# Kernel tuning notes

Hardware: AMD Instinct MI355X
Metric: run time of the kernel (lower is better)

Reference implementation:

```python
import jax, jax.numpy as jnp
import numpy as np

N, E, F_IN, HID, H1, H2, H3, OUT = 10000, 160000, 50, 350, 4, 4, 6, 121


def _gat(x, src, dst, n, W, a_s, a_d, b, heads, C, concat):
    # PyG GATConv (dropout=0, eval): h = xW^T reshaped to [N,H,C]
    h = (x @ W.T).reshape(n, heads, C)
    alpha_src = jnp.einsum('nhc,hc->nh', h, a_s)  # [N,H]
    alpha_dst = jnp.einsum('nhc,hc->nh', h, a_d)  # [N,H]
    e = jax.nn.leaky_relu(alpha_src[src] + alpha_dst[dst], 0.2)  # [E,H]
    # numerically-stable segment softmax over incoming edges of each dst node
    m = jax.ops.segment_max(e, dst, num_segments=n)
    ee = jnp.exp(e - m[dst])
    s = jax.ops.segment_sum(ee, dst, num_segments=n)
    alpha = ee / s[dst]  # self-loops guarantee s > 0
    out = jax.ops.segment_sum(h[src] * alpha[:, :, None], dst, num_segments=n)  # [N,H,C]
    out = out.reshape(n, heads * C) if concat else out.mean(axis=1)
    return out + b


def setup_inputs() -> dict:
    key = jax.random.key(0)
    ks = jax.random.split(key, 16)
    sc = 0.05
    inp = {
        'x': jax.random.normal(ks[0], (N, F_IN), dtype=jnp.float32),
        'edge_index': jax.random.randint(ks[1], (2, E), 0, N, dtype=jnp.int64) if jax.config.jax_enable_x64 else jax.random.randint(ks[1], (2, E), 0, N, dtype=jnp.int32),
        'W1': jax.random.normal(ks[2], (H1 * HID, F_IN), dtype=jnp.float32) * sc,
        'a1s': jax.random.normal(ks[3], (H1, HID), dtype=jnp.float32) * sc,
        'a1d': jax.random.normal(ks[4], (H1, HID), dtype=jnp.float32) * sc,
        'b1': jnp.zeros((H1 * HID,), dtype=jnp.float32),
        'W2': jax.random.normal(ks[5], (H2 * HID, H1 * HID), dtype=jnp.float32) * sc,
        'a2s': jax.random.normal(ks[6], (H2, HID), dtype=jnp.float32) * sc,
        'a2d': jax.random.normal(ks[7], (H2, HID), dtype=jnp.float32) * sc,
        'b2': jnp.zeros((H2 * HID,), dtype=jnp.float32),
        'Wskip': jax.random.normal(ks[8], (H2 * HID, H1 * HID), dtype=jnp.float32) * sc,
        'W3': jax.random.normal(ks[9], (H3 * OUT, H2 * HID), dtype=jnp.float32) * sc,
        'a3s': jax.random.normal(ks[10], (H3, OUT), dtype=jnp.float32) * sc,
        'a3d': jax.random.normal(ks[11], (H3, OUT), dtype=jnp.float32) * sc,
        'b3': jnp.zeros((OUT,), dtype=jnp.float32),
    }
    return inp


def reference(x, edge_index, W1, a1s, a1d, b1, W2, a2s, a2d, b2, Wskip, W3, a3s, a3d, b3):
    n = x.shape[0]
    loops = jnp.arange(n, dtype=edge_index.dtype)  # PyG add_self_loops=True
    src = jnp.concatenate([edge_index[0], loops])
    dst = jnp.concatenate([edge_index[1], loops])
    h = jax.nn.elu(_gat(x, src, dst, n, W1, a1s, a1d, b1, H1, HID, True))
    x_in = h
    h = jax.nn.elu(_gat(h, src, dst, n, W2, a2s, a2d, b2, H2, HID, True))
    h = h + x_in @ Wskip.T  # skip connection (bias=False)
    return _gat(h, src, dst, n, W3, a3s, a3d, b3, H3, OUT, False)
```

## Files before the change

kernel.cpp:

```cpp
#include <hip/hip_runtime.h>
#include <math.h>

#define NNODES 10000
#define NEDGES 160000
#define E2 (NEDGES + NNODES)
#define F_IN 50
#define HIDC 350
#define NH1 4
#define NH2 4
#define NH3 6
#define OUTC 121
#define MAXE 96
#define KP1 64
#define KP2 1408
#define LD3 736
#define ROWSLACK 128

typedef __attribute__((ext_vector_type(8))) short short8;
typedef __attribute__((ext_vector_type(8))) unsigned short ushort8v;
typedef __attribute__((ext_vector_type(4))) float floatx4;

static __device__ __forceinline__ unsigned short f2bf(float f) {
    unsigned u = __float_as_uint(f);
    unsigned r = (u + 0x7fffu + ((u >> 16) & 1u)) >> 16;
    return (unsigned short)r;
}
static __device__ __forceinline__ float bf2f(unsigned short s) {
    return __uint_as_float(((unsigned)s) << 16);
}

#define GLL16(gp, lp)                                                      \
    __builtin_amdgcn_global_load_lds(                                      \
        (const __attribute__((address_space(1))) void*)(gp),               \
        (__attribute__((address_space(3))) void*)(lp), 16, 0, 0)

__global__ void count_kernel(const int* __restrict__ ei, int* __restrict__ cnt) {
    int i = blockIdx.x * blockDim.x + threadIdx.x;
    if (i >= E2) return;
    int dst = (i < NEDGES) ? ei[NEDGES + i] : (i - NEDGES);
    atomicAdd(&cnt[dst], 1);
}

__global__ void scan_kernel(const int* __restrict__ cnt, int* __restrict__ indptr,
                            int* __restrict__ cursor) {
    __shared__ int part[1024];
    int tid = threadIdx.x;
    const int CH = (NNODES + 1023) / 1024;
    int base = tid * CH;
    int s = 0;
    for (int i = 0; i < CH; i++) {
        int idx = base + i;
        if (idx < NNODES) s += cnt[idx];
    }
    part[tid] = s;
    __syncthreads();
    for (int off = 1; off < 1024; off <<= 1) {
        int v = (tid >= off) ? part[tid - off] : 0;
        __syncthreads();
        part[tid] += v;
        __syncthreads();
    }
    int run = (tid == 0) ? 0 : part[tid - 1];
    for (int i = 0; i < CH; i++) {
        int idx = base + i;
        if (idx < NNODES) {
            indptr[idx] = run;
            cursor[idx] = run;
            run += cnt[idx];
        }
    }
    if (tid == 0) indptr[NNODES] = part[1023];
}

__global__ void scatter_kernel(const int* __restrict__ ei, int* __restrict__ cursor,
                               int* __restrict__ esrc) {
    int i = blockIdx.x * blockDim.x + threadIdx.x;
    if (i >= E2) return;
    int src, dst;
    if (i < NEDGES) {
        src = ei[i];
        dst = ei[NEDGES + i];
    } else {
        src = dst = i - NEDGES;
    }
    int pos = atomicAdd(&cursor[dst], 1);
    esrc[pos] = src;
}

__global__ void splitW1_kernel(const float* __restrict__ W1,
                               unsigned short* __restrict__ w1Hi,
                               unsigned short* __restrict__ w1Lo) {
    int k = threadIdx.x;
    int r = blockIdx.x;
    float v = (k < F_IN) ? W1[(size_t)r * F_IN + k] : 0.f;
    unsigned short h = f2bf(v);
    w1Hi[(size_t)r * KP1 + k] = h;
    w1Lo[(size_t)r * KP1 + k] = f2bf(v - bf2f(h));
}

__global__ void splitB_kernel(const float* __restrict__ W2, const float* __restrict__ Wsk,
                              const float* __restrict__ W3,
                              unsigned short* __restrict__ w2Hi,
                              unsigned short* __restrict__ w3Hi) {
    int k = blockIdx.x * blockDim.x + threadIdx.x;
    if (k >= KP2) return;
    int r = blockIdx.y;
    const int K = 1400;
    const float* src;
    unsigned short* hi;
    int row;
    if (r < 1400) { src = W2; row = r; hi = w2Hi; }
    else if (r < 2800) { src = Wsk; row = r - 1400; hi = w2Hi + (size_t)1400 * KP2; }
    else { src = W3; row = r - 2800; hi = w3Hi; }
    float v = (k < K) ? src[(size_t)row * K + k] : 0.f;
    hi[(size_t)row * KP2 + k] = f2bf(v);
}

__global__ void atil_kernel(const float* __restrict__ W, const float* __restrict__ av_s,
                            const float* __restrict__ av_d, float* __restrict__ outS,
                            float* __restrict__ outD, int C, int K, int cchunk) {
    int k = blockIdx.x * 64 + (threadIdx.x & 63);
    if (k >= K) return;
    int h = blockIdx.y;
    int c0 = blockIdx.z * cchunk;
    int c1 = c0 + cchunk;
    if (c1 > C) c1 = C;
    float ss = 0.f, dd = 0.f;
    for (int c = c0; c < c1; c++) {
        float wv = W[((size_t)h * C + c) * K + k];
        ss = fmaf(wv, av_s[h * C + c], ss);
        dd = fmaf(wv, av_d[h * C + c], dd);
    }
    atomicAdd(&outS[(size_t)h * K + k], ss);
    atomicAdd(&outD[(size_t)h * K + k], dd);
}

__global__ void splitAT2_kernel(const float* __restrict__ atall,
                                unsigned short* __restrict__ atHi,
                                unsigned short* __restrict__ atLo) {
    int k = blockIdx.x * 64 + threadIdx.x;
    int r = blockIdx.y;
    float v = 0.f;
    if (k < 1400) {
        if (r < 4) v = atall[400 + r * 1400 + k];
        else if (r < 8) v = atall[6000 + (r - 4) * 1400 + k];
    }
    unsigned short h = f2bf(v);
    atHi[(size_t)r * KP2 + k] = h;
    atLo[(size_t)r * KP2 + k] = f2bf(v - bf2f(h));
}

__global__ __launch_bounds__(256) void alpha1x_kernel(const float* __restrict__ x,
                                                      const float* __restrict__ at1s,
                                                      const float* __restrict__ at1d,
                                                      float* __restrict__ as1,
                                                      float* __restrict__ ad1) {
    int wave = threadIdx.x >> 6, lane = threadIdx.x & 63;
    int n = blockIdx.x * 4 + wave;
    if (n >= NNODES) return;
    int kk = lane < F_IN ? lane : F_IN - 1;
    float v = (lane < F_IN) ? x[(size_t)n * F_IN + lane] : 0.f;
    float p[8];
#pragma unroll
    for (int h = 0; h < 4; h++) {
        p[h] = v * at1s[h * F_IN + kk];
        p[4 + h] = v * at1d[h * F_IN + kk];
    }
#pragma unroll
    for (int s = 0; s < 8; s++)
#pragma unroll
        for (int o = 32; o > 0; o >>= 1) p[s] += __shfl_xor(p[s], o, 64);
    if (lane == 0) {
#pragma unroll
        for (int h = 0; h < 4; h++) {
            as1[n * 4 + h] = p[h];
            ad1[n * 4 + h] = p[4 + h];
        }
    }
}

__global__ void zeropad_kernel(unsigned short* __restrict__ hi) {
    int i = blockIdx.x * 256 + threadIdx.x;
    if (i >= NNODES * 8) return;
    int n = i >> 3, c = 1400 + (i & 7);
    hi[(size_t)n * KP2 + c] = 0;
}

__global__ __launch_bounds__(256) void agg_x(
    const float* __restrict__ x, const float* __restrict__ as_n,
    const float* __restrict__ ad_n, const int* __restrict__ indptr,
    const int* __restrict__ esrc, unsigned short* __restrict__ xaggHi,
    unsigned short* __restrict__ xaggLo) {
    int n = blockIdx.x, tid = threadIdx.x;
    int s = indptr[n], e = indptr[n + 1];
    int deg = e - s;
    if (deg > MAXE) deg = MAXE;
    __shared__ int srcs[MAXE];
    __shared__ float wgt[MAXE * 4];

    if (tid < 64) {
        int lane = tid;
        float adv[4], mx[4], sm[4];
#pragma unroll
        for (int h = 0; h < 4; h++) {
            adv[h] = ad_n[n * 4 + h];
            mx[h] = -1e30f;
            sm[h] = 0.f;
        }
        for (int j = lane; j < deg; j += 64) {
            int sr = esrc[s + j];
            srcs[j] = sr;
#pragma unroll
            for (int h = 0; h < 4; h++) {
                float ev = as_n[sr * 4 + h] + adv[h];
                ev = ev > 0.f ? ev : 0.2f * ev;
                wgt[j * 4 + h] = ev;
                mx[h] = fmaxf(mx[h], ev);
            }
        }
#pragma unroll
        for (int h = 0; h < 4; h++)
#pragma unroll
            for (int o = 32; o > 0; o >>= 1) mx[h] = fmaxf(mx[h], __shfl_xor(mx[h], o, 64));
        for (int j = lane; j < deg; j += 64) {
#pragma unroll
            for (int h = 0; h < 4; h++) {
                float p = __expf(wgt[j * 4 + h] - mx[h]);
                wgt[j * 4 + h] = p;
                sm[h] += p;
            }
        }
#pragma unroll
        for (int h = 0; h < 4; h++) {
#pragma unroll
            for (int o = 32; o > 0; o >>= 1) sm[h] += __shfl_xor(sm[h], o, 64);
            sm[h] = 1.f / sm[h];
        }
        for (int j = lane; j < deg; j += 64) {
#pragma unroll
            for (int h = 0; h < 4; h++) wgt[j * 4 + h] *= sm[h];
        }
    }
    __syncthreads();

    int h = tid >> 6, k = tid & 63;
    float a = 0.f;
    if (k < F_IN) {
        float a2 = 0.f;
        int j = 0;
        for (; j + 1 < deg; j += 2) {
            a = fmaf(wgt[j * 4 + h], x[(size_t)srcs[j] * F_IN + k], a);
            a2 = fmaf(wgt[(j + 1) * 4 + h], x[(size_t)srcs[j + 1] * F_IN + k], a2);
        }
        if (j < deg) a = fmaf(wgt[j * 4 + h], x[(size_t)srcs[j] * F_IN + k], a);
        a += a2;
    }
    unsigned short hi = f2bf(a);
    xaggHi[(size_t)n * 256 + tid] = hi;
    xaggLo[(size_t)n * 256 + tid] = f2bf(a - bf2f(hi));
}

__global__ __launch_bounds__(256, 2) void gemm_h1(
    const unsigned short* __restrict__ xaggHi, const unsigned short* __restrict__ xaggLo,
    const unsigned short* __restrict__ w1Hi, const unsigned short* __restrict__ w1Lo,
    const float* __restrict__ bias, unsigned short* __restrict__ actHi) {
    __shared__ __align__(16) unsigned short sA[2][128 * 32];
    __shared__ __align__(16) unsigned short sB[2][256 * 32];
    int tid = threadIdx.x;
    int wave = tid >> 6, lane = tid & 63;
    int wm = (wave >> 1) * 64, wn = (wave & 1) * 128;
    int fr = lane & 15, kq = lane >> 4;
    int row0 = blockIdx.y * 128, col0 = blockIdx.x * 256;
    int hd = blockIdx.z;

    floatx4 acc[4][8];
#pragma unroll
    for (int i = 0; i < 4; i++)
#pragma unroll
        for (int j = 0; j < 8; j++)
#pragma unroll
            for (int q = 0; q < 4; q++) acc[i][j][q] = 0.f;

    int gpos = lane & 3;
    int rl = lane >> 2;
    int gsw = kq ^ ((fr >> 1) & 3);

    for (int k0 = 0; k0 < 64; k0 += 32) {
#pragma unroll
        for (int c = 0; c < 2; ++c) {
            int r = wave * 32 + c * 16 + rl;
            int g = gpos ^ ((r >> 1) & 3);
            size_t gofs = (size_t)(row0 + r) * 256 + hd * 64 + k0 + g * 8;
            size_t lofs = (size_t)r * 32 + (size_t)gpos * 8;
            GLL16(xaggHi + gofs, &sA[0][lofs]);
            GLL16(xaggLo + gofs, &sA[1][lofs]);
        }
#pragma unroll
        for (int c = 0; c < 4; ++c) {
            int r = wave * 64 + c * 16 + rl;
            int g = gpos ^ ((r >> 1) & 3);
            size_t gofs = (size_t)(hd * 350 + col0 + r) * KP1 + k0 + g * 8;
            size_t lofs = (size_t)r * 32 + (size_t)gpos * 8;
            GLL16(w1Hi + gofs, &sB[0][lofs]);
            GLL16(w1Lo + gofs, &sB[1][lofs]);
        }
        __syncthreads();

        short8 ah[4], al[4], bh[8], bl[8];
#pragma unroll
        for (int j = 0; j < 8; j++) {
            int rb = wn + j * 16 + fr;
            bh[j] = *(const short8*)&sB[0][rb * 32 + gsw * 8];
            bl[j] = *(const short8*)&sB[1][rb * 32 + gsw * 8];
        }
#pragma unroll
        for (int i = 0; i < 4; i++) {
            int ra = wm + i * 16 + fr;
            ah[i] = *(const short8*)&sA[0][ra * 32 + gsw * 8];
            al[i] = *(const short8*)&sA[1][ra * 32 + gsw * 8];
        }
#pragma unroll
        for (int i = 0; i < 4; i++)
#pragma unroll
            for (int j = 0; j < 8; j++) {
                acc[i][j] = __builtin_amdgcn_mfma_f32_16x16x32_bf16(ah[i], bh[j],
                                                                   acc[i][j], 0, 0, 0);
                acc[i][j] = __builtin_amdgcn_mfma_f32_16x16x32_bf16(al[i], bh[j],
                                                                   acc[i][j], 0, 0, 0);
                acc[i][j] = __builtin_amdgcn_mfma_f32_16x16x32_bf16(ah[i], bl[j],
                                                                   acc[i][j], 0, 0, 0);
            }
        __syncthreads();
    }

#pragma unroll
    for (int i = 0; i < 4; i++) {
#pragma unroll
        for (int rg = 0; rg < 4; rg++) {
            int rr = row0 + wm + i * 16 + kq * 4 + rg;
            if (rr >= NNODES) continue;
#pragma unroll
            for (int j = 0; j < 8; j++) {
                int cc = col0 + wn + j * 16 + fr;
                if (cc < 350) {
                    int gc = hd * 350 + cc;
                    float v = acc[i][j][rg] + bias[gc];
                    v = v > 0.f ? v : expm1f(v);
                    actHi[(size_t)rr * KP2 + gc] = f2bf(v);
                }
            }
        }
    }
}

__global__ __launch_bounds__(256) void alpha_mfma(
    const unsigned short* __restrict__ act, const unsigned short* __restrict__ tHi,
    const unsigned short* __restrict__ tLo, int H, float* __restrict__ asx,
    float* __restrict__ adx) {
    int wave = threadIdx.x >> 6, lane = threadIdx.x & 63;
    int row0 = (blockIdx.x * 4 + wave) * 16;
    if (row0 >= NNODES) return;
    int fr = lane & 15, kq = lane >> 4;
    floatx4 acc = {0.f, 0.f, 0.f, 0.f};
    const unsigned short* arow = act + (size_t)(row0 + fr) * KP2 + kq * 8;
    const unsigned short* brh = tHi + (size_t)fr * KP2 + kq * 8;
    const unsigned short* brl = tLo + (size_t)fr * KP2 + kq * 8;
#pragma unroll 4
    for (int k0 = 0; k0 < KP2; k0 += 32) {
        short8 a = *(const short8*)(arow + k0);
        short8 vh = *(const short8*)(brh + k0);
        short8 vl = *(const short8*)(brl + k0);
        acc = __builtin_amdgcn_mfma_f32_16x16x32_bf16(a, vh, acc, 0, 0, 0);
        acc = __builtin_amdgcn_mfma_f32_16x16x32_bf16(a, vl, acc, 0, 0, 0);
    }
#pragma unroll
    for (int rg = 0; rg < 4; rg++) {
        int rr = row0 + kq * 4 + rg;
        if (fr < H) asx[rr * H + fr] = acc[rg];
        else if (fr < 2 * H) adx[rr * H + (fr - H)] = acc[rg];
    }
}

__global__ __launch_bounds__(256, 2) void gemm_b16(
    const unsigned short* __restrict__ A, const unsigned short* __restrict__ B,
    unsigned short* __restrict__ Cb, int NN, int M, int Kp, int ldc) {
    __shared__ __align__(16) unsigned short sA[128 * 32];
    __shared__ __align__(16) unsigned short sB[256 * 32];
    int tid = threadIdx.x;
    int wave = tid >> 6, lane = tid & 63;
    int wm = (wave >> 1) * 64, wn = (wave & 1) * 128;
    int fr = lane & 15, kq = lane >> 4;
    int row0 = blockIdx.y * 128, col0 = blockIdx.x * 256;

    floatx4 acc[4][8];
#pragma unroll
    for (int i = 0; i < 4; i++)
#pragma unroll
        for (int j = 0; j < 8; j++)
#pragma unroll
            for (int q = 0; q < 4; q++) acc[i][j][q] = 0.f;

    int gpos = lane & 3;
    int rl = lane >> 2;
    int gsw = kq ^ ((fr >> 1) & 3);

    for (int k0 = 0; k0 < Kp; k0 += 32) {
#pragma unroll
        for (int c = 0; c < 2; ++c) {
            int r = wave * 32 + c * 16 + rl;
            int g = gpos ^ ((r >> 1) & 3);
            GLL16(A + (size_t)(row0 + r) * Kp + k0 + g * 8,
                  &sA[(size_t)r * 32 + (size_t)gpos * 8]);
        }
#pragma unroll
        for (int c = 0; c < 4; ++c) {
            int r = wave * 64 + c * 16 + rl;
            int g = gpos ^ ((r >> 1) & 3);
            GLL16(B + (size_t)(col0 + r) * Kp + k0 + g * 8,
                  &sB[(size_t)r * 32 + (size_t)gpos * 8]);
        }
        __syncthreads();

        short8 ah[4], bh[8];
#pragma unroll
        for (int j = 0; j < 8; j++) {
            int rb = wn + j * 16 + fr;
            bh[j] = *(const short8*)&sB[rb * 32 + gsw * 8];
        }
#pragma unroll
        for (int i = 0; i < 4; i++) {
            int ra = wm + i * 16 + fr;
            ah[i] = *(const short8*)&sA[ra * 32 + gsw * 8];
        }
#pragma unroll
        for (int i = 0; i < 4; i++)
#pragma unroll
            for (int j = 0; j < 8; j++)
                acc[i][j] = __builtin_amdgcn_mfma_f32_16x16x32_bf16(ah[i], bh[j],
                                                                   acc[i][j], 0, 0, 0);
        __syncthreads();
    }

#pragma unroll
    for (int i = 0; i < 4; i++) {
#pragma unroll
        for (int rg = 0; rg < 4; rg++) {
            int rr = row0 + wm + i * 16 + kq * 4 + rg;
            if (rr >= NN) continue;
#pragma unroll
            for (int j = 0; j < 8; j++) {
                int cc = col0 + wn + j * 16 + fr;
                if (cc < M) Cb[(size_t)rr * ldc + cc] = f2bf(acc[i][j][rg]);
            }
        }
    }
}

#define AGG_T 192
template <int H, int C, int MODE, int DOELU, int SKIP, int HN>
__global__ __launch_bounds__(AGG_T) void agg2(
    const unsigned short* __restrict__ hpreb, int ldh,
    const float* __restrict__ as_n, const float* __restrict__ ad_n,
    const int* __restrict__ indptr, const int* __restrict__ esrc,
    const float* __restrict__ bias, unsigned short* __restrict__ outHi, int Kp,
    float* __restrict__ outF, const float* __restrict__ atns,
    const float* __restrict__ atnd, float* __restrict__ asx,
    float* __restrict__ adx) {
    constexpr int HC = H * C;
    int n = blockIdx.x;
    int tid = threadIdx.x;
    int s = indptr[n], e = indptr[n + 1];
    int deg = e - s;
    if (deg > MAXE) deg = MAXE;

    __shared__ int srcs[MAXE];
    __shared__ float wgt[MAXE * H];
    __shared__ float aggsh[MODE ? HC : 1];
    __shared__ float sAl[16];
    if (tid < 16) sAl[tid] = 0.f;

    if (tid < 64) {
        int lane = tid;
        float adv[H], mx[H], sm[H];
#pragma unroll
        for (int h = 0; h < H; h++) {
            adv[h] = ad_n[n * H + h];
            mx[h] = -1e30f;
            sm[h] = 0.f;
        }
        for (int j = lane; j < deg; j += 64) {
            int sr = esrc[s + j];
            srcs[j] = sr;
#pragma unroll
            for (int h = 0; h < H; h++) {
                float ev = as_n[sr * H + h] + adv[h];
                ev = ev > 0.f ? ev : 0.2f * ev;
                wgt[j * H + h] = ev;
                mx[h] = fmaxf(mx[h], ev);
            }
        }
#pragma unroll
        for (int h = 0; h < H; h++)
#pragma unroll
            for (int o = 32; o > 0; o >>= 1) mx[h] = fmaxf(mx[h], __shfl_xor(mx[h], o, 64));
        for (int j = lane; j < deg; j += 64) {
#pragma unroll
            for (int h = 0; h < H; h++) {
                float p = __expf(wgt[j * H + h] - mx[h]);
                wgt[j * H + h] = p;
                sm[h] += p;
            }
        }
#pragma unroll
        for (int h = 0; h < H; h++) {
#pragma unroll
            for (int o = 32; o > 0; o >>= 1) sm[h] += __shfl_xor(sm[h], o, 64);
            sm[h] = 1.f / sm[h];
        }
        for (int j = lane; j < deg; j += 64) {
#pragma unroll
            for (int h = 0; h < H; h++) wgt[j * H + h] *= sm[h];
        }
    }
    __syncthreads();

    if (MODE == 0) {
        constexpr int NV8 = HC / 8;
        constexpr int NP = (HN > 0) ? 2 * HN : 1;
        float p[NP];
#pragma unroll
        for (int q = 0; q < NP; q++) p[q] = 0.f;

        for (int c8 = tid; c8 < NV8; c8 += AGG_T) {
            int cb = c8 * 8;
            int h0 = cb / C;
            int sp = (h0 + 1) * C - cb;
            if (sp > 8) sp = 8;
            int h1 = (h0 + 1 < H) ? h0 + 1 : h0;
            float av[8];
#pragma unroll
            for (int q = 0; q < 8; q++) av[q] = 0.f;
            int j = 0;
            for (; j + 3 < deg; j += 4) {
                const ushort8v v0 = *(const ushort8v*)(hpreb + (size_t)srcs[j] * ldh + cb);
                const ushort8v v1 = *(const ushort8v*)(hpreb + (size_t)srcs[j + 1] * ldh + cb);
                const ushort8v v2 = *(const ushort8v*)(hpreb + (size_t)srcs[j + 2] * ldh + cb);
                const ushort8v v3 = *(const ushort8v*)(hpreb + (size_t)srcs[j + 3] * ldh + cb);
                float wa0 = wgt[j * H + h0], wa1 = wgt[j * H + h1];
                float wb0 = wgt[(j + 1) * H + h0], wb1 = wgt[(j + 1) * H + h1];
                float wc0 = wgt[(j + 2) * H + h0], wc1 = wgt[(j + 2) * H + h1];
                float wd0 = wgt[(j + 3) * H + h0], wd1 = wgt[(j + 3) * H + h1];
#pragma unroll
                for (int q = 0; q < 8; q++) av[q] = fmaf(q < sp ? wa0 : wa1, bf2f(v0[q]), av[q]);
#pragma unroll
                for (int q = 0; q < 8; q++) av[q] = fmaf(q < sp ? wb0 : wb1, bf2f(v1[q]), av[q]);
#pragma unroll
                for (int q = 0; q < 8; q++) av[q] = fmaf(q < sp ? wc0 : wc1, bf2f(v2[q]), av[q]);
#pragma unroll
                for (int q = 0; q < 8; q++) av[q] = fmaf(q < sp ? wd0 : wd1, bf2f(v3[q]), av[q]);
            }
            for (; j < deg; j++) {
                const ushort8v v0 = *(const ushort8v*)(hpreb + (size_t)srcs[j] * ldh + cb);
                float wa0 = wgt[j * H + h0], wa1 = wgt[j * H + h1];
#pragma unroll
                for (int q = 0; q < 8; q++) av[q] = fmaf(q < sp ? wa0 : wa1, bf2f(v0[q]), av[q]);
            }
#pragma unroll
            for (int q = 0; q < 8; q++) av[q] += bias[cb + q];
            if (DOELU) {
#pragma unroll
                for (int q = 0; q < 8; q++) av[q] = av[q] > 0.f ? av[q] : expm1f(av[q]);
            }
            if (SKIP) {
                const ushort8v sk = *(const ushort8v*)(hpreb + (size_t)n * ldh + 1400 + cb);
#pragma unroll
                for (int q = 0; q < 8; q++) av[q] += bf2f(sk[q]);
            }
            if (HN > 0) {
#pragma unroll
                for (int h = 0; h < HN; h++) {
                    float ss = 0.f, dd = 0.f;
#pragma unroll
                    for (int q = 0; q < 8; q++) {
                        ss = fmaf(av[q], atns[(size_t)h * HC + cb + q], ss);
                        dd = fmaf(av[q], atnd[(size_t)h * HC + cb + q], dd);
                    }
                    p[h] += ss;
                    p[HN + h] += dd;
                }
            }
            ushort8v hi8;
#pragma unroll
            for (int q = 0; q < 8; q++) hi8[q] = f2bf(av[q]);
            *(ushort8v*)(outHi + (size_t)n * Kp + cb) = hi8;
        }
        for (int c = HC + tid; c < Kp; c += AGG_T) outHi[(size_t)n * Kp + c] = 0;
        if (HN > 0) {
#pragma unroll
            for (int q = 0; q < NP; q++)
#pragma unroll
                for (int o = 32; o > 0; o >>= 1) p[q] += __shfl_xor(p[q], o, 64);
            if ((tid & 63) == 0) {
#pragma unroll
                for (int q = 0; q < NP; q++) atomicAdd(&sAl[q], p[q]);
            }
            __syncthreads();
            if (tid < HN) asx[n * HN + tid] = sAl[tid];
            else if (tid < 2 * HN) adx[n * HN + (tid - HN)] = sAl[tid];
        }
    } else {
        constexpr int NV8 = (HC + 7) / 8;
        for (int c8 = tid; c8 < NV8; c8 += AGG_T) {
            int cb = c8 * 8;
            int h0 = cb / C;
            if (h0 >= H) h0 = H - 1;
            int sp = (h0 + 1) * C - cb;
            if (sp > 8) sp = 8;
            int h1 = (h0 + 1 < H) ? h0 + 1 : h0;
            float av[8];
#pragma unroll
            for (int q = 0; q < 8; q++) av[q] = 0.f;
            int j = 0;
            for (; j + 3 < deg; j += 4) {
                const ushort8v v0 = *(const ushort8v*)(hpreb + (size_t)srcs[j] * ldh + cb);
                const ushort8v v1 = *(const ushort8v*)(hpreb + (size_t)srcs[j + 1] * ldh + cb);
                const ushort8v v2 = *(const ushort8v*)(hpreb + (size_t)srcs[j + 2] * ldh + cb);
                const ushort8v v3 = *(const ushort8v*)(hpreb + (size_t)srcs[j + 3] * ldh + cb);
                float wa0 = wgt[j * H + h0], wa1 = wgt[j * H + h1];
                float wb0 = wgt[(j + 1) * H + h0], wb1 = wgt[(j + 1) * H + h1];
                float wc0 = wgt[(j + 2) * H + h0], wc1 = wgt[(j + 2) * H + h1];
                float wd0 = wgt[(j + 3) * H + h0], wd1 = wgt[(j + 3) * H + h1];
#pragma unroll
                for (int q = 0; q < 8; q++) av[q] = fmaf(q < sp ? wa0 : wa1, bf2f(v0[q]), av[q]);
#pragma unroll
                for (int q = 0; q < 8; q++) av[q] = fmaf(q < sp ? wb0 : wb1, bf2f(v1[q]), av[q]);
#pragma unroll
                for (int q = 0; q < 8; q++) av[q] = fmaf(q < sp ? wc0 : wc1, bf2f(v2[q]), av[q]);
#pragma unroll
                for (int q = 0; q < 8; q++) av[q] = fmaf(q < sp ? wd0 : wd1, bf2f(v3[q]), av[q]);
            }
            for (; j < deg; j++) {
                const ushort8v v0 = *(const ushort8v*)(hpreb + (size_t)srcs[j] * ldh + cb);
                float wa0 = wgt[j * H + h0], wa1 = wgt[j * H + h1];
#pragma unroll
                for (int q = 0; q < 8; q++) av[q] = fmaf(q < sp ? wa0 : wa1, bf2f(v0[q]), av[q]);
            }
#pragma unroll
            for (int q = 0; q < 8; q++)
                if (cb + q < HC) aggsh[cb + q] = av[q];
        }
        __syncthreads();
        for (int c = tid; c < C; c += AGG_T) {
            float sres = 0.f;
#pragma unroll
            for (int h = 0; h < H; h++) sres += aggsh[h * C + c];
            outF[(size_t)n * C + c] = sres * (1.f / (float)H) + bias[c];
        }
    }
}

extern "C" void kernel_launch(void* const* d_in, const int* in_sizes, int n_in,
                              void* d_out, int out_size, void* d_ws, size_t ws_size,
                              hipStream_t stream) {
    const float* x = (const float*)d_in[0];
    const int* ei = (const int*)d_in[1];
    const float* W1 = (const float*)d_in[2];
    const float* a1s = (const float*)d_in[3];
    const float* a1d = (const float*)d_in[4];
    const float* b1 = (const float*)d_in[5];
    const float* W2 = (const float*)d_in[6];
    const float* a2s = (const float*)d_in[7];
    const float* a2d = (const float*)d_in[8];
    const float* b2 = (const float*)d_in[9];
    const float* Wsk = (const float*)d_in[10];
    const float* W3 = (const float*)d_in[11];
    const float* a3s = (const float*)d_in[12];
    const float* a3d = (const float*)d_in[13];
    const float* b3 = (const float*)d_in[14];
    float* out = (float*)d_out;

    char* w = (char*)d_ws;
    size_t off = 0;
    auto alloc = [&](size_t bytes) -> char* {
        char* p = w + off;
        off += (bytes + 255) & ~(size_t)255;
        return p;
    };
    unsigned short* hpreb = (unsigned short*)alloc((size_t)(NNODES + ROWSLACK) * 2800 * 2);
    unsigned short* actHi = (unsigned short*)alloc((size_t)(NNODES + ROWSLACK) * KP2 * 2);
    unsigned short* xaggHi = (unsigned short*)alloc((size_t)(NNODES + ROWSLACK) * 256 * 2);
    unsigned short* xaggLo = (unsigned short*)alloc((size_t)(NNODES + ROWSLACK) * 256 * 2);
    unsigned short* w1Hi = (unsigned short*)alloc((size_t)(1400 + 512) * KP1 * 2);
    unsigned short* w1Lo = (unsigned short*)alloc((size_t)(1400 + 512) * KP1 * 2);
    unsigned short* w2Hi = (unsigned short*)alloc((size_t)(2800 + ROWSLACK) * KP2 * 2);
    unsigned short* w3Hi = (unsigned short*)alloc((size_t)(726 + ROWSLACK) * KP2 * 2);
    unsigned short* at2Hi = (unsigned short*)alloc((size_t)16 * KP2 * 2);
    unsigned short* at2Lo = (unsigned short*)alloc((size_t)16 * KP2 * 2);
    float* atall = (float*)alloc((size_t)28400 * 4);
    int* cnt = (int*)alloc((size_t)(NNODES + 16) * 4);
    float* at1s = atall;
    float* at1d = atall + 200;
    float* at2s = atall + 400;
    float* at2d = atall + 6000;
    float* at3s = atall + 11600;
    float* at3d = atall + 20000;
    float* asP = (float*)alloc((size_t)NNODES * 6 * 4);
    float* adP = (float*)alloc((size_t)NNODES * 6 * 4);
    float* asQ = (float*)alloc((size_t)NNODES * 6 * 4);
    float* adQ = (float*)alloc((size_t)NNODES * 6 * 4);
    int* indptr = (int*)alloc((size_t)(NNODES + 16) * 4);
    int* cursor = (int*)alloc((size_t)(NNODES + 16) * 4);
    int* esrc = (int*)alloc((size_t)E2 * 4);

    size_t zbytes = (size_t)((char*)cnt - (char*)atall) + (NNODES + 16) * 4;
    hipMemsetAsync(atall, 0, zbytes, stream);

    splitW1_kernel<<<1400, 64, 0, stream>>>(W1, w1Hi, w1Lo);
    splitB_kernel<<<dim3(6, 2800 + 726), 256, 0, stream>>>(W2, Wsk, W3, w2Hi, w3Hi);
    atil_kernel<<<dim3(1, 4, 5), 64, 0, stream>>>(W1, a1s, a1d, at1s, at1d, HIDC, F_IN, 70);
    atil_kernel<<<dim3(22, 4, 5), 64, 0, stream>>>(W2, a2s, a2d, at2s, at2d, HIDC, 1400, 70);
    atil_kernel<<<dim3(22, 6, 4), 64, 0, stream>>>(W3, a3s, a3d, at3s, at3d, OUTC, 1400, 31);
    splitAT2_kernel<<<dim3(22, 16), 64, 0, stream>>>(atall, at2Hi, at2Lo);
    alpha1x_kernel<<<(NNODES + 3) / 4, 256, 0, stream>>>(x, at1s, at1d, asP, adP);

    count_kernel<<<(E2 + 255) / 256, 256, 0, stream>>>(ei, cnt);
    scan_kernel<<<1, 1024, 0, stream>>>(cnt, indptr, cursor);
    scatter_kernel<<<(E2 + 255) / 256, 256, 0, stream>>>(ei, cursor, esrc);

    zeropad_kernel<<<(NNODES * 8 + 255) / 256, 256, 0, stream>>>(actHi);

    dim3 blk(256);
    int gy = (NNODES + 127) / 128;

    agg_x<<<NNODES, 256, 0, stream>>>(x, asP, adP, indptr, esrc, xaggHi, xaggLo);
    gemm_h1<<<dim3(2, gy, 4), blk, 0, stream>>>(xaggHi, xaggLo, w1Hi, w1Lo, b1, actHi);
    alpha_mfma<<<(NNODES / 16 + 3) / 4, 256, 0, stream>>>(actHi, at2Hi, at2Lo, 4, asQ, adQ);

    {
        int M = 2800;
        dim3 grid((M + 255) / 256, gy);
        gemm_b16<<<grid, blk, 0, stream>>>(actHi, w2Hi, hpreb, NNODES, M, KP2, 2800);
        agg2<NH2, HIDC, 0, 1, 1, 6><<<NNODES, AGG_T, 0, stream>>>(
            hpreb, 2800, asQ, adQ, indptr, esrc, b2, actHi, KP2, nullptr,
            at3s, at3d, asP, adP);
    }
    {
        int M = NH3 * OUTC;
        dim3 grid((M + 255) / 256, gy);
        gemm_b16<<<grid, blk, 0, stream>>>(actHi, w3Hi, hpreb, NNODES, M, KP2, LD3);
        agg2<NH3, OUTC, 1, 0, 0, 0><<<NNODES, AGG_T, 0, stream>>>(
            hpreb, LD3, asP, adP, indptr, esrc, b3, nullptr, 0, out,
            nullptr, nullptr, nullptr, nullptr);
    }
}
```

Measured before the change: 635.1 us.

## Chunk layer-2 features by column slabs and aggregate 8 nodes per block

The layer-2 GEMM now writes its output into 8 column-chunked slabs (176 columns each) plus a separate skip region. A new aggregation kernel has each block handle one chunk for 8 nodes, so the gathered rows within a block share a narrower slab and should get better cache locality. Softmax edge weights are precomputed once by a separate kernel and stored per edge. Per-chunk partial layer-3 attention logits go to a buffer that an extra reduce kernel sums. This adds two kernels and extra global traffic for the edge weights and partials.

```diff
diff --git a/kernel.cpp b/kernel.cpp
--- a/kernel.cpp
+++ b/kernel.cpp
@@ -15,6 +15,9 @@
 #define KP2 1408
 #define LD3 736
 #define ROWSLACK 128
+#define GCH 176
+#define GSL ((size_t)NNODES * GCH)
+#define HSKOFF ((size_t)8 * GSL)
 
 typedef __attribute__((ext_vector_type(8))) short short8;
 typedef __attribute__((ext_vector_type(8))) unsigned short ushort8v;
@@ -381,9 +384,63 @@
     }
 }
 
+__global__ __launch_bounds__(64) void alpha_edge4(
+    const float* __restrict__ as_n, const float* __restrict__ ad_n,
+    const int* __restrict__ indptr, const int* __restrict__ esrc,
+    float* __restrict__ walpha) {
+    int n = blockIdx.x;
+    int lane = threadIdx.x;
+    int s = indptr[n], e = indptr[n + 1];
+    int deg = e - s;
+    if (deg > MAXE) deg = MAXE;
+    __shared__ float wgt[MAXE * 4];
+    float adv[4], mx[4], sm[4];
+#pragma unroll
+    for (int h = 0; h < 4; h++) {
+        adv[h] = ad_n[n * 4 + h];
+        mx[h] = -1e30f;
+        sm[h] = 0.f;
+    }
+    for (int j = lane; j < deg; j += 64) {
+        int sr = esrc[s + j];
+#pragma unroll
+        for (int h = 0; h < 4; h++) {
+            float ev = as_n[sr * 4 + h] + adv[h];
+            ev = ev > 0.f ? ev : 0.2f * ev;
+            wgt[j * 4 + h] = ev;
+            mx[h] = fmaxf(mx[h], ev);
+        }
+    }
+#pragma unroll
+    for (int h = 0; h < 4; h++)
+#pragma unroll
+        for (int o = 32; o > 0; o >>= 1) mx[h] = fmaxf(mx[h], __shfl_xor(mx[h], o, 64));
+    for (int j = lane; j < deg; j += 64) {
+#pragma unroll
+        for (int h = 0; h < 4; h++) {
+            float p = __expf(wgt[j * 4 + h] - mx[h]);
+            wgt[j * 4 + h] = p;
+            sm[h] += p;
+        }
+    }
+#pragma unroll
+    for (int h = 0; h < 4; h++) {
+#pragma unroll
+        for (int o = 32; o > 0; o >>= 1) sm[h] += __shfl_xor(sm[h], o, 64);
+        sm[h] = 1.f / sm[h];
+    }
+    for (int j = lane; j < deg; j += 64) {
+#pragma unroll
+        for (int h = 0; h < 4; h++) wgt[j * 4 + h] *= sm[h];
+    }
+    __syncthreads();
+    for (int i = lane; i < deg * 4; i += 64)
+        walpha[(size_t)s * 4 + i] = wgt[i];
+}
+
 __global__ __launch_bounds__(256, 2) void gemm_b16(
     const unsigned short* __restrict__ A, const unsigned short* __restrict__ B,
-    unsigned short* __restrict__ Cb, int NN, int M, int Kp, int ldc) {
+    unsigned short* __restrict__ Cb, int NN, int M, int Kp, int ldc, int wmode) {
     __shared__ __align__(16) unsigned short sA[128 * 32];
     __shared__ __align__(16) unsigned short sB[256 * 32];
     int tid = threadIdx.x;
@@ -450,22 +507,162 @@
 #pragma unroll
             for (int j = 0; j < 8; j++) {
                 int cc = col0 + wn + j * 16 + fr;
-                if (cc < M) Cb[(size_t)rr * ldc + cc] = f2bf(acc[i][j][rg]);
-            }
-        }
-    }
+                if (cc < M) {
+                    unsigned short val = f2bf(acc[i][j][rg]);
+                    if (wmode == 0) {
+                        Cb[(size_t)rr * ldc + cc] = val;
+                    } else if (cc < 1400) {
+                        int ch = cc / GCH;
+                        int off = cc - ch * GCH;
+                        Cb[(size_t)ch * GSL + (size_t)rr * GCH + off] = val;
+                    } else {
+                        Cb[HSKOFF + (size_t)rr * 1408 + (cc - 1400)] = val;
+                    }
+                }
+            }
+        }
+    }
+}
+
+__global__ __launch_bounds__(192) void agg2c(
+    const unsigned short* __restrict__ hbuf, const int* __restrict__ indptr,
+    const int* __restrict__ esrc, const float* __restrict__ walpha,
+    const float* __restrict__ bias, unsigned short* __restrict__ outHi,
+    const float* __restrict__ atns, const float* __restrict__ atnd,
+    float* __restrict__ a3part) {
+    int c = blockIdx.x & 7;
+    int g = blockIdx.x >> 3;
+    int tid = threadIdx.x;
+
+    __shared__ int sS[8][MAXE];
+    __shared__ float sW[8][MAXE * 4];
+    __shared__ float part[176][13];
+    __shared__ int sDeg[8];
+
+    {
+        int nn = tid / 24, l = tid - nn * 24;
+        int n = g * 8 + nn;
+        int s = indptr[n];
+        int deg = indptr[n + 1] - s;
+        if (deg > MAXE) deg = MAXE;
+        if (l == 0) sDeg[nn] = deg;
+        for (int i = l; i < deg; i += 24)
+            sS[nn][i] = __builtin_nontemporal_load(esrc + s + i);
+        for (int i = l; i < deg * 4; i += 24)
+            sW[nn][i] = __builtin_nontemporal_load(walpha + (size_t)s * 4 + i);
+    }
+    __syncthreads();
+
+    float p[12];
+#pragma unroll
+    for (int q = 0; q < 12; q++) p[q] = 0.f;
+
+    if (tid < 176) {
+        int nn = tid / 22, u = tid - nn * 22;
+        int n = g * 8 + nn;
+        int cb = (c * 22 + u) * 8;
+        if (cb < 1400) {
+            int deg = sDeg[nn];
+            int h0 = cb / 350;
+            int sp = (h0 + 1) * 350 - cb;
+            if (sp > 8) sp = 8;
+            int h1 = (h0 + 1 < 4) ? h0 + 1 : h0;
+            const float* w = sW[nn];
+            const int* sl = sS[nn];
+            const unsigned short* base = hbuf + (size_t)c * GSL + (size_t)u * 8;
+            float av[8];
+#pragma unroll
+            for (int q = 0; q < 8; q++) av[q] = 0.f;
+            int j = 0;
+            for (; j + 3 < deg; j += 4) {
+                const ushort8v v0 = *(const ushort8v*)(base + (size_t)sl[j] * GCH);
+                const ushort8v v1 = *(const ushort8v*)(base + (size_t)sl[j + 1] * GCH);
+                const ushort8v v2 = *(const ushort8v*)(base + (size_t)sl[j + 2] * GCH);
+                const ushort8v v3 = *(const ushort8v*)(base + (size_t)sl[j + 3] * GCH);
+                float wa0 = w[j * 4 + h0], wa1 = w[j * 4 + h1];
+                float wb0 = w[(j + 1) * 4 + h0], wb1 = w[(j + 1) * 4 + h1];
+                float wc0 = w[(j + 2) * 4 + h0], wc1 = w[(j + 2) * 4 + h1];
+                float wd0 = w[(j + 3) * 4 + h0], wd1 = w[(j + 3) * 4 + h1];
+#pragma unroll
+                for (int q = 0; q < 8; q++) av[q] = fmaf(q < sp ? wa0 : wa1, bf2f(v0[q]), av[q]);
+#pragma unroll
+                for (int q = 0; q < 8; q++) av[q] = fmaf(q < sp ? wb0 : wb1, bf2f(v1[q]), av[q]);
+#pragma unroll
+                for (int q = 0; q < 8; q++) av[q] = fmaf(q < sp ? wc0 : wc1, bf2f(v2[q]), av[q]);
+#pragma unroll
+                for (int q = 0; q < 8; q++) av[q] = fmaf(q < sp ? wd0 : wd1, bf2f(v3[q]), av[q]);
+            }
+            for (; j < deg; j++) {
+                const ushort8v v0 = *(const ushort8v*)(base + (size_t)sl[j] * GCH);
+                float wa0 = w[j * 4 + h0], wa1 = w[j * 4 + h1];
+#pragma unroll
+                for (int q = 0; q < 8; q++) av[q] = fmaf(q < sp ? wa0 : wa1, bf2f(v0[q]), av[q]);
+            }
+#pragma unroll
+            for (int q = 0; q < 8; q++) av[q] += bias[cb + q];
+#pragma unroll
+            for (int q = 0; q < 8; q++) av[q] = av[q] > 0.f ? av[q] : expm1f(av[q]);
+            const ushort8v sk = __builtin_nontemporal_load(
+                (const ushort8v*)(hbuf + HSKOFF + (size_t)n * 1408 + cb));
+#pragma unroll
+            for (int q = 0; q < 8; q++) av[q] += bf2f(sk[q]);
+#pragma unroll
+            for (int h = 0; h < 6; h++) {
+                float ss = 0.f, dd = 0.f;
+#pragma unroll
+                for (int q = 0; q < 8; q++) {
+                    ss = fmaf(av[q], atns[(size_t)h * 1400 + cb + q], ss);
+                    dd = fmaf(av[q], atnd[(size_t)h * 1400 + cb + q], dd);
+                }
+                p[h] = ss;
+                p[6 + h] = dd;
+            }
+            ushort8v hi8;
+#pragma unroll
+            for (int q = 0; q < 8; q++) hi8[q] = f2bf(av[q]);
+            __builtin_nontemporal_store(hi8, (ushort8v*)(outHi + (size_t)n * KP2 + cb));
+        } else {
+            ushort8v z;
+#pragma unroll
+            for (int q = 0; q < 8; q++) z[q] = 0;
+            __builtin_nontemporal_store(z, (ushort8v*)(outHi + (size_t)n * KP2 + cb));
+        }
+#pragma unroll
+        for (int q = 0; q < 12; q++) part[tid][q] = p[q];
+    }
+    __syncthreads();
+    if (tid < 96) {
+        int nn = tid / 12, q = tid - nn * 12;
+        float sres = 0.f;
+        const float* pp = &part[nn * 22][q];
+#pragma unroll
+        for (int u = 0; u < 22; u++) sres += pp[u * 13];
+        int n = g * 8 + nn;
+        a3part[(size_t)n * 96 + c * 12 + q] = sres;
+    }
+}
+
+__global__ __launch_bounds__(256) void a3reduce(const float* __restrict__ a3part,
+                                                float* __restrict__ asx,
+                                                float* __restrict__ adx) {
+    int t = blockIdx.x * 256 + threadIdx.x;
+    if (t >= NNODES * 12) return;
+    int n = t / 12, q = t - n * 12;
+    const float* pp = a3part + (size_t)n * 96 + q;
+    float s = 0.f;
+#pragma unroll
+    for (int c = 0; c < 8; c++) s += pp[c * 12];
+    if (q < 6) asx[n * 6 + q] = s;
+    else adx[n * 6 + (q - 6)] = s;
 }
 
 #define AGG_T 192
-template <int H, int C, int MODE, int DOELU, int SKIP, int HN>
-__global__ __launch_bounds__(AGG_T) void agg2(
+template <int H, int C>
+__global__ __launch_bounds__(AGG_T) void agg3(
     const unsigned short* __restrict__ hpreb, int ldh,
     const float* __restrict__ as_n, const float* __restrict__ ad_n,
     const int* __restrict__ indptr, const int* __restrict__ esrc,
-    const float* __restrict__ bias, unsigned short* __restrict__ outHi, int Kp,
-    float* __restrict__ outF, const float* __restrict__ atns,
-    const float* __restrict__ atnd, float* __restrict__ asx,
-    float* __restrict__ adx) {
+    const float* __restrict__ bias, float* __restrict__ outF) {
     constexpr int HC = H * C;
     int n = blockIdx.x;
     int tid = threadIdx.x;
@@ -475,9 +672,7 @@
 
     __shared__ int srcs[MAXE];
     __shared__ float wgt[MAXE * H];
-    __shared__ float aggsh[MODE ? HC : 1];
-    __shared__ float sAl[16];
-    if (tid < 16) sAl[tid] = 0.f;
+    __shared__ float aggsh[HC];
 
     if (tid < 64) {
         int lane = tid;
@@ -524,138 +719,52 @@
     }
     __syncthreads();
 
-    if (MODE == 0) {
-        constexpr int NV8 = HC / 8;
-        constexpr int NP = (HN > 0) ? 2 * HN : 1;
-        float p[NP];
-#pragma unroll
-        for (int q = 0; q < NP; q++) p[q] = 0.f;
-
-        for (int c8 = tid; c8 < NV8; c8 += AGG_T) {
-            int cb = c8 * 8;
-            int h0 = cb / C;
-            int sp = (h0 + 1) * C - cb;
-            if (sp > 8) sp = 8;
-            int h1 = (h0 + 1 < H) ? h0 + 1 : h0;
-            float av[8];
-#pragma unroll
-            for (int q = 0; q < 8; q++) av[q] = 0.f;
-            int j = 0;
-            for (; j + 3 < deg; j += 4) {
-                const ushort8v v0 = *(const ushort8v*)(hpreb + (size_t)srcs[j] * ldh + cb);
-                const ushort8v v1 = *(const ushort8v*)(hpreb + (size_t)srcs[j + 1] * ldh + cb);
-                const ushort8v v2 = *(const ushort8v*)(hpreb + (size_t)srcs[j + 2] * ldh + cb);
-                const ushort8v v3 = *(const ushort8v*)(hpreb + (size_t)srcs[j + 3] * ldh + cb);
-                float wa0 = wgt[j * H + h0], wa1 = wgt[j * H + h1];
-                float wb0 = wgt[(j + 1) * H + h0], wb1 = wgt[(j + 1) * H + h1];
-                float wc0 = wgt[(j + 2) * H + h0], wc1 = wgt[(j + 2) * H + h1];
-                float wd0 = wgt[(j + 3) * H + h0], wd1 = wgt[(j + 3) * H + h1];
-#pragma unroll
-                for (int q = 0; q < 8; q++) av[q] = fmaf(q < sp ? wa0 : wa1, bf2f(v0[q]), av[q]);
-#pragma unroll
-                for (int q = 0; q < 8; q++) av[q] = fmaf(q < sp ? wb0 : wb1, bf2f(v1[q]), av[q]);
-#pragma unroll
-                for (int q = 0; q < 8; q++) av[q] = fmaf(q < sp ? wc0 : wc1, bf2f(v2[q]), av[q]);
-#pragma unroll
-                for (int q = 0; q < 8; q++) av[q] = fmaf(q < sp ? wd0 : wd1, bf2f(v3[q]), av[q]);
-            }
-            for (; j < deg; j++) {
-                const ushort8v v0 = *(const ushort8v*)(hpreb + (size_t)srcs[j] * ldh + cb);
-                float wa0 = wgt[j * H + h0], wa1 = wgt[j * H + h1];
-#pragma unroll
-                for (int q = 0; q < 8; q++) av[q] = fmaf(q < sp ? wa0 : wa1, bf2f(v0[q]), av[q]);
-            }
-#pragma unroll
-            for (int q = 0; q < 8; q++) av[q] += bias[cb + q];
-            if (DOELU) {
-#pragma unroll
-                for (int q = 0; q < 8; q++) av[q] = av[q] > 0.f ? av[q] : expm1f(av[q]);
-            }
-            if (SKIP) {
-                const ushort8v sk = *(const ushort8v*)(hpreb + (size_t)n * ldh + 1400 + cb);
-#pragma unroll
-                for (int q = 0; q < 8; q++) av[q] += bf2f(sk[q]);
-            }
-            if (HN > 0) {
-#pragma unroll
-                for (int h = 0; h < HN; h++) {
-                    float ss = 0.f, dd = 0.f;
-#pragma unroll
-                    for (int q = 0; q < 8; q++) {
-                        ss = fmaf(av[q], atns[(size_t)h * HC + cb + q], ss);
-                        dd = fmaf(av[q], atnd[(size_t)h * HC + cb + q], dd);
-                    }
-                    p[h] += ss;
-                    p[HN + h] += dd;
-                }
-            }
-            ushort8v hi8;
-#pragma unroll
-            for (int q = 0; q < 8; q++) hi8[q] = f2bf(av[q]);
-            *(ushort8v*)(outHi + (size_t)n * Kp + cb) = hi8;
-        }
-        for (int c = HC + tid; c < Kp; c += AGG_T) outHi[(size_t)n * Kp + c] = 0;
-        if (HN > 0) {
-#pragma unroll
-            for (int q = 0; q < NP; q++)
-#pragma unroll
-                for (int o = 32; o > 0; o >>= 1) p[q] += __shfl_xor(p[q], o, 64);
-            if ((tid & 63) == 0) {
-#pragma unroll
-                for (int q = 0; q < NP; q++) atomicAdd(&sAl[q], p[q]);
-            }
-            __syncthreads();
-            if (tid < HN) asx[n * HN + tid] = sAl[tid];
-            else if (tid < 2 * HN) adx[n * HN + (tid - HN)] = sAl[tid];
-        }
-    } else {
-        constexpr int NV8 = (HC + 7) / 8;
-        for (int c8 = tid; c8 < NV8; c8 += AGG_T) {
-            int cb = c8 * 8;
-            int h0 = cb / C;
-            if (h0 >= H) h0 = H - 1;
-            int sp = (h0 + 1) * C - cb;
-            if (sp > 8) sp = 8;
-            int h1 = (h0 + 1 < H) ? h0 + 1 : h0;
-            float av[8];
-#pragma unroll
-            for (int q = 0; q < 8; q++) av[q] = 0.f;
-            int j = 0;
-            for (; j + 3 < deg; j += 4) {
-                const ushort8v v0 = *(const ushort8v*)(hpreb + (size_t)srcs[j] * ldh + cb);
-                const ushort8v v1 = *(const ushort8v*)(hpreb + (size_t)srcs[j + 1] * ldh + cb);
-                const ushort8v v2 = *(const ushort8v*)(hpreb + (size_t)srcs[j + 2] * ldh + cb);
-                const ushort8v v3 = *(const ushort8v*)(hpreb + (size_t)srcs[j + 3] * ldh + cb);
-                float wa0 = wgt[j * H + h0], wa1 = wgt[j * H + h1];
-                float wb0 = wgt[(j + 1) * H + h0], wb1 = wgt[(j + 1) * H + h1];
-                float wc0 = wgt[(j + 2) * H + h0], wc1 = wgt[(j + 2) * H + h1];
-                float wd0 = wgt[(j + 3) * H + h0], wd1 = wgt[(j + 3) * H + h1];
-#pragma unroll
-                for (int q = 0; q < 8; q++) av[q] = fmaf(q < sp ? wa0 : wa1, bf2f(v0[q]), av[q]);
-#pragma unroll
-                for (int q = 0; q < 8; q++) av[q] = fmaf(q < sp ? wb0 : wb1, bf2f(v1[q]), av[q]);
-#pragma unroll
-                for (int q = 0; q < 8; q++) av[q] = fmaf(q < sp ? wc0 : wc1, bf2f(v2[q]), av[q]);
-#pragma unroll
-                for (int q = 0; q < 8; q++) av[q] = fmaf(q < sp ? wd0 : wd1, bf2f(v3[q]), av[q]);
-            }
-            for (; j < deg; j++) {
-                const ushort8v v0 = *(const ushort8v*)(hpreb + (size_t)srcs[j] * ldh + cb);
-                float wa0 = wgt[j * H + h0], wa1 = wgt[j * H + h1];
-#pragma unroll
-                for (int q = 0; q < 8; q++) av[q] = fmaf(q < sp ? wa0 : wa1, bf2f(v0[q]), av[q]);
-            }
-#pragma unroll
-            for (int q = 0; q < 8; q++)
-                if (cb + q < HC) aggsh[cb + q] = av[q];
-        }
-        __syncthreads();
-        for (int c = tid; c < C; c += AGG_T) {
-            float sres = 0.f;
-#pragma unroll
-            for (int h = 0; h < H; h++) sres += aggsh[h * C + c];
-            outF[(size_t)n * C + c] = sres * (1.f / (float)H) + bias[c];
-        }
+    constexpr int NV8 = (HC + 7) / 8;
+    for (int c8 = tid; c8 < NV8; c8 += AGG_T) {
+        int cb = c8 * 8;
+        int h0 = cb / C;
+        if (h0 >= H) h0 = H - 1;
+        int sp = (h0 + 1) * C - cb;
+        if (sp > 8) sp = 8;
+        int h1 = (h0 + 1 < H) ? h0 + 1 : h0;
+        float av[8];
+#pragma unroll
+        for (int q = 0; q < 8; q++) av[q] = 0.f;
+        int j = 0;
+        for (; j + 3 < deg; j += 4) {
+            const ushort8v v0 = *(const ushort8v*)(hpreb + (size_t)srcs[j] * ldh + cb);
+            const ushort8v v1 = *(const ushort8v*)(hpreb + (size_t)srcs[j + 1] * ldh + cb);
+            const ushort8v v2 = *(const ushort8v*)(hpreb + (size_t)srcs[j + 2] * ldh + cb);
+            const ushort8v v3 = *(const ushort8v*)(hpreb + (size_t)srcs[j + 3] * ldh + cb);
+            float wa0 = wgt[j * H + h0], wa1 = wgt[j * H + h1];
+            float wb0 = wgt[(j + 1) * H + h0], wb1 = wgt[(j + 1) * H + h1];
+            float wc0 = wgt[(j + 2) * H + h0], wc1 = wgt[(j + 2) * H + h1];
+            float wd0 = wgt[(j + 3) * H + h0], wd1 = wgt[(j + 3) * H + h1];
+#pragma unroll
+            for (int q = 0; q < 8; q++) av[q] = fmaf(q < sp ? wa0 : wa1, bf2f(v0[q]), av[q]);
+#pragma unroll
+            for (int q = 0; q < 8; q++) av[q] = fmaf(q < sp ? wb0 : wb1, bf2f(v1[q]), av[q]);
+#pragma unroll
+            for (int q = 0; q < 8; q++) av[q] = fmaf(q < sp ? wc0 : wc1, bf2f(v2[q]), av[q]);
+#pragma unroll
+            for (int q = 0; q < 8; q++) av[q] = fmaf(q < sp ? wd0 : wd1, bf2f(v3[q]), av[q]);
+        }
+        for (; j < deg; j++) {
+            const ushort8v v0 = *(const ushort8v*)(hpreb + (size_t)srcs[j] * ldh + cb);
+            float wa0 = wgt[j * H + h0], wa1 = wgt[j * H + h1];
+#pragma unroll
+            for (int q = 0; q < 8; q++) av[q] = fmaf(q < sp ? wa0 : wa1, bf2f(v0[q]), av[q]);
+        }
+#pragma unroll
+        for (int q = 0; q < 8; q++)
+            if (cb + q < HC) aggsh[cb + q] = av[q];
+    }
+    __syncthreads();
+    for (int c = tid; c < C; c += AGG_T) {
+        float sres = 0.f;
+#pragma unroll
+        for (int h = 0; h < H; h++) sres += aggsh[h * C + c];
+        outF[(size_t)n * C + c] = sres * (1.f / (float)H) + bias[c];
     }
 }
 
@@ -711,6 +820,8 @@
     int* indptr = (int*)alloc((size_t)(NNODES + 16) * 4);
     int* cursor = (int*)alloc((size_t)(NNODES + 16) * 4);
     int* esrc = (int*)alloc((size_t)E2 * 4);
+    float* walpha = (float*)alloc((size_t)E2 * 4 * 4);
+    float* a3part = (float*)alloc((size_t)NNODES * 96 * 4);
 
     size_t zbytes = (size_t)((char*)cnt - (char*)atall) + (NNODES + 16) * 4;
     hipMemsetAsync(atall, 0, zbytes, stream);
@@ -735,21 +846,21 @@
     agg_x<<<NNODES, 256, 0, stream>>>(x, asP, adP, indptr, esrc, xaggHi, xaggLo);
     gemm_h1<<<dim3(2, gy, 4), blk, 0, stream>>>(xaggHi, xaggLo, w1Hi, w1Lo, b1, actHi);
     alpha_mfma<<<(NNODES / 16 + 3) / 4, 256, 0, stream>>>(actHi, at2Hi, at2Lo, 4, asQ, adQ);
+    alpha_edge4<<<NNODES, 64, 0, stream>>>(asQ, adQ, indptr, esrc, walpha);
 
     {
         int M = 2800;
         dim3 grid((M + 255) / 256, gy);
-        gemm_b16<<<grid, blk, 0, stream>>>(actHi, w2Hi, hpreb, NNODES, M, KP2, 2800);
-        agg2<NH2, HIDC, 0, 1, 1, 6><<<NNODES, AGG_T, 0, stream>>>(
-            hpreb, 2800, asQ, adQ, indptr, esrc, b2, actHi, KP2, nullptr,
-            at3s, at3d, asP, adP);
+        gemm_b16<<<grid, blk, 0, stream>>>(actHi, w2Hi, hpreb, NNODES, M, KP2, 2800, 1);
+        agg2c<<<NNODES, 192, 0, stream>>>(hpreb, indptr, esrc, walpha, b2, actHi,
+                                          at3s, at3d, a3part);
+        a3reduce<<<(NNODES * 12 + 255) / 256, 256, 0, stream>>>(a3part, asP, adP);
     }
     {
         int M = NH3 * OUTC;
         dim3 grid((M + 255) / 256, gy);
-        gemm_b16<<<grid, blk, 0, stream>>>(actHi, w3Hi, hpreb, NNODES, M, KP2, LD3);
-        agg2<NH3, OUTC, 1, 0, 0, 0><<<NNODES, AGG_T, 0, stream>>>(
-            hpreb, LD3, asP, adP, indptr, esrc, b3, nullptr, 0, out,
-            nullptr, nullptr, nullptr, nullptr);
-    }
-}
+        gemm_b16<<<grid, blk, 0, stream>>>(actHi, w3Hi, hpreb, NNODES, M, KP2, LD3, 0);
+        agg3<NH3, OUTC><<<NNODES, AGG_T, 0, stream>>>(
+            hpreb, LD3, asP, adP, indptr, esrc, b3, out);
+    }
+}
```

After: 655.5 us. 3.2% more time.
